# Optimization experiments

Measured on AMD Instinct MI355X. Metric: run time of the kernel, lower is better.

Reference implementation:

```python
import jax, jax.numpy as jnp
import numpy as np

N = 20000
E = 320000
IN_C = 256
HID = 64
OUT_C = 64
NUM_LAYERS = 3
HEADS = 8


def setup_inputs() -> dict:
    key = jax.random.key(0)
    ks = jax.random.split(key, 12)
    s_in = 1.0 / np.sqrt(IN_C)
    s_h = 1.0 / np.sqrt(HID)
    inp = {
        "x": jax.random.normal(ks[0], (N, IN_C), dtype=jnp.float32),
        "edge_index": jax.random.randint(ks[1], (2, E), 0, N, dtype=jnp.int64),
        "lin1_w": jax.random.uniform(ks[2], (IN_C, HID), jnp.float32, -s_in, s_in),
        "lin1_b": jnp.zeros((HID,), jnp.float32),
        "wq": jax.random.uniform(ks[3], (NUM_LAYERS, HID, HID), jnp.float32, -s_h, s_h),
        "bq": jnp.zeros((NUM_LAYERS, HID), jnp.float32),
        "wk": jax.random.uniform(ks[4], (NUM_LAYERS, HID, HID), jnp.float32, -s_h, s_h),
        "bk": jnp.zeros((NUM_LAYERS, HID), jnp.float32),
        "wv": jax.random.uniform(ks[5], (NUM_LAYERS, HID, HID), jnp.float32, -s_h, s_h),
        "bv": jnp.zeros((NUM_LAYERS, HID), jnp.float32),
        "lin2_w": jax.random.uniform(ks[6], (HID, OUT_C), jnp.float32, -s_h, s_h),
        "lin2_b": jnp.zeros((OUT_C,), jnp.float32),
    }
    return inp


def reference(x, edge_index, lin1_w, lin1_b, wq, bq, wk, bk, wv, bv, lin2_w, lin2_b):
    n = x.shape[0]
    C = lin1_w.shape[1]
    d = C // HEADS  # per-head dim
    inv_sqrt_d = 1.0 / (d ** 0.5)

    # gcn_norm with self-loops (symmetric normalization, edge weights = 1)
    loop = jnp.arange(n, dtype=edge_index.dtype)
    row = jnp.concatenate([edge_index[0], loop])  # source j
    col = jnp.concatenate([edge_index[1], loop])  # target i
    deg = jax.ops.segment_sum(jnp.ones_like(col, dtype=x.dtype), col, num_segments=n)
    dinv = jnp.where(deg > 0, deg ** -0.5, 0.0)
    norm = dinv[row] * dinv[col]  # [E+N]

    # input projection (dropout inactive in eval mode)
    h = jax.nn.relu(x @ lin1_w + lin1_b)
    x_all = h[:, None, :]  # [N, 1, C] growing history

    for l in range(NUM_LAYERS):
        t = x_all.shape[1]
        # node-level projections (linear commutes with gather)
        q = x_all[:, -1] @ wq[l] + bq[l]                      # [N, C]
        k = jnp.einsum("ntc,cd->ntd", x_all, wk[l]) + bk[l]   # [N, t, C]
        v = jnp.einsum("ntc,cd->ntd", x_all, wv[l]) + bv[l]   # [N, t, C]
        # per-edge multi-head attention of target's latest repr over source history
        Qe = q[col].reshape(-1, HEADS, d)                      # [E', H, d]
        Ke = k[row].reshape(-1, t, HEADS, d)                   # [E', t, H, d]
        Ve = v[row].reshape(-1, t, HEADS, d)
        scores = jnp.einsum("ehd,ethd->eht", Qe, Ke) * inv_sqrt_d
        attn = jax.nn.softmax(scores, axis=-1)                 # [E', H, t]
        msg = jnp.einsum("eht,ethd->ehd", attn, Ve).reshape(-1, C)
        msg = msg * norm[:, None]
        out = jax.ops.segment_sum(msg, col, num_segments=n)    # sum aggregation
        out = jax.nn.relu(out)
        x_all = jnp.concatenate([x_all, out[:, None, :]], axis=1)

    logits = x_all[:, -1] @ lin2_w + lin2_b
    return jax.nn.log_softmax(logits, axis=1)
```

## Files before the change

### kernel.cpp

```cpp
#include <hip/hip_runtime.h>
#include <math.h>

#define HID 64
#define HEADS 8
#define NUM_LAYERS 3

__device__ __forceinline__ unsigned short f2bf(float f) {
    union { float f; unsigned int u; } cv; cv.f = f;
    unsigned int u = cv.u;
    unsigned int r = (u + 0x7FFFu + ((u >> 16) & 1u)) >> 16;
    return (unsigned short)r;
}
__device__ __forceinline__ float bflo(unsigned int u) {
    union { unsigned int u; float f; } cv; cv.u = u << 16; return cv.f;
}
__device__ __forceinline__ float bfhi(unsigned int u) {
    union { unsigned int u; float f; } cv; cv.u = u & 0xFFFF0000u; return cv.f;
}

__global__ void k_count(const int* __restrict__ col, int* __restrict__ counts, int E) {
    int e = blockIdx.x * blockDim.x + threadIdx.x;
    if (e < E) atomicAdd(&counts[col[e]], 1);
}

__global__ __launch_bounds__(1024) void k_scan(const int* __restrict__ counts,
                                               int* __restrict__ start,
                                               float* __restrict__ dinv, int n) {
    __shared__ int wsum[16];
    __shared__ int carry_s;
    int tid = threadIdx.x;
    int lane = tid & 63, wv = tid >> 6;
    if (tid == 0) carry_s = 0;
    __syncthreads();
    for (int base = 0; base < n; base += 1024) {
        int i = base + tid;
        int v = (i < n) ? counts[i] : 0;
        int x = v;
#pragma unroll
        for (int off = 1; off < 64; off <<= 1) {
            int y = __shfl_up(x, off);
            if (lane >= off) x += y;
        }
        if (lane == 63) wsum[wv] = x;
        __syncthreads();
        if (wv == 0 && lane < 16) {
            int s = wsum[lane];
#pragma unroll
            for (int off = 1; off < 16; off <<= 1) {
                int y = __shfl_up(s, off);
                if (lane >= off) s += y;
            }
            wsum[lane] = s;
        }
        __syncthreads();
        int waveoff = (wv > 0) ? wsum[wv - 1] : 0;
        int carry = carry_s;
        if (i < n) {
            start[i] = carry + waveoff + x - v;
            dinv[i] = rsqrtf((float)(v + 1));
        }
        __syncthreads();
        if (tid == 0) carry_s = carry + wsum[15];
        __syncthreads();
    }
    if (threadIdx.x == 0) start[n] = carry_s;
}

__global__ void k_scatter(const int* __restrict__ ei, const int* __restrict__ start,
                          int* __restrict__ fill, int* __restrict__ ebuf, int E) {
    int e = blockIdx.x * blockDim.x + threadIdx.x;
    if (e >= E) return;
    int r = ei[e], c = ei[E + e];
    int pos = start[c] + atomicAdd(&fill[c], 1);
    ebuf[pos] = r;
}

#define ST_STRIDE 68

__device__ __forceinline__ void gemm_tile_stage_src(
    float* st, const float* __restrict__ src, int node0, int n, int ld,
    int kc, bool relu_in, int tid) {
    int nd = tid >> 4;
    int c4 = (tid & 15) * 4;
#pragma unroll
    for (int rep = 0; rep < 4; ++rep) {
        int lnode = nd + rep * 16;
        int node = node0 + lnode;
        float4 v = make_float4(0.f, 0.f, 0.f, 0.f);
        if (node < n) v = *(const float4*)&src[(size_t)node * ld + kc + c4];
        if (relu_in) {
            v.x = fmaxf(v.x, 0.f); v.y = fmaxf(v.y, 0.f);
            v.z = fmaxf(v.z, 0.f); v.w = fmaxf(v.w, 0.f);
        }
        st[(c4 + 0) * ST_STRIDE + lnode] = v.x;
        st[(c4 + 1) * ST_STRIDE + lnode] = v.y;
        st[(c4 + 2) * ST_STRIDE + lnode] = v.z;
        st[(c4 + 3) * ST_STRIDE + lnode] = v.w;
    }
}

__device__ __forceinline__ void gemm_tile_inner(
    const float* st, const float* wl, int ri, int j, float acc[4][4]) {
#pragma unroll 4
    for (int c = 0; c < 64; ++c) {
        float4 a  = *(const float4*)&st[c * ST_STRIDE + ri * 4];
        float4 b4 = *(const float4*)&wl[c * 64 + j * 4];
        acc[0][0] += a.x * b4.x; acc[0][1] += a.x * b4.y;
        acc[0][2] += a.x * b4.z; acc[0][3] += a.x * b4.w;
        acc[1][0] += a.y * b4.x; acc[1][1] += a.y * b4.y;
        acc[1][2] += a.y * b4.z; acc[1][3] += a.y * b4.w;
        acc[2][0] += a.z * b4.x; acc[2][1] += a.z * b4.y;
        acc[2][2] += a.z * b4.z; acc[2][3] += a.z * b4.w;
        acc[3][0] += a.w * b4.x; acc[3][1] += a.w * b4.y;
        acc[3][2] += a.w * b4.z; acc[3][3] += a.w * b4.w;
    }
}

__global__ __launch_bounds__(256, 4) void k_lin1(const float* __restrict__ x,
                                                 const float* __restrict__ w,
                                                 const float* __restrict__ b,
                                                 float* __restrict__ h, int n) {
    __shared__ float wl[64 * 64];
    __shared__ float st[64 * ST_STRIDE];
    int tid = threadIdx.x;
    int node0 = blockIdx.x * 64;
    int ri = tid >> 4, j = tid & 15;
    float acc[4][4];
#pragma unroll
    for (int m = 0; m < 4; ++m)
#pragma unroll
        for (int k = 0; k < 4; ++k) acc[m][k] = 0.f;

    for (int kc = 0; kc < 256; kc += 64) {
        for (int i = tid * 4; i < 4096; i += 1024)
            *(float4*)&wl[i] = *(const float4*)&w[kc * 64 + i];
        gemm_tile_stage_src(st, x, node0, n, 256, kc, false, tid);
        __syncthreads();
        gemm_tile_inner(st, wl, ri, j, acc);
        __syncthreads();
    }
    float4 bb = *(const float4*)&b[j * 4];
#pragma unroll
    for (int m = 0; m < 4; ++m) {
        int node = node0 + ri * 4 + m;
        if (node < n) {
            float4 o = make_float4(fmaxf(acc[m][0] + bb.x, 0.f),
                                   fmaxf(acc[m][1] + bb.y, 0.f),
                                   fmaxf(acc[m][2] + bb.z, 0.f),
                                   fmaxf(acc[m][3] + bb.w, 0.f));
            *(float4*)&h[(size_t)node * 64 + j * 4] = o;
        }
    }
}

__global__ __launch_bounds__(256, 4) void k_qkv(
    const float* __restrict__ xsbase,
    const float* __restrict__ wq, const float* __restrict__ bq,
    const float* __restrict__ wk, const float* __restrict__ bk,
    const float* __restrict__ wv, const float* __restrict__ bv,
    float* __restrict__ q, unsigned short* __restrict__ kv,
    int n, int layer, int t, int job_offset, int kv_stride) {
    int job = blockIdx.y + job_offset;
    const float* src; const float* w; const float* b; bool relu_in;
    int kv_off = 0;
    if (job == 0) {
        src = xsbase + (size_t)layer * n * 64;
        w = wq + layer * 4096; b = bq + layer * 64;
        relu_in = (layer >= 1);
    } else if (job <= t) {
        int s = job - 1;
        src = xsbase + (size_t)s * n * 64;
        w = wk + layer * 4096; b = bk + layer * 64;
        kv_off = s * 128;
        relu_in = (s >= 1);
    } else {
        int s = job - t - 1;
        src = xsbase + (size_t)s * n * 64;
        w = wv + layer * 4096; b = bv + layer * 64;
        kv_off = (t == 1) ? 0 : s * 128 + 64;
        relu_in = (s >= 1);
    }
    __shared__ float wl[64 * 64];
    __shared__ float st[64 * ST_STRIDE];
    int tid = threadIdx.x;
    int node0 = blockIdx.x * 64;
    for (int i = tid * 4; i < 4096; i += 1024)
        *(float4*)&wl[i] = *(const float4*)&w[i];
    gemm_tile_stage_src(st, src, node0, n, 64, 0, relu_in, tid);
    __syncthreads();
    int ri = tid >> 4, j = tid & 15;
    float acc[4][4];
#pragma unroll
    for (int m = 0; m < 4; ++m)
#pragma unroll
        for (int k = 0; k < 4; ++k) acc[m][k] = 0.f;
    gemm_tile_inner(st, wl, ri, j, acc);
    float4 bb = *(const float4*)&b[j * 4];
    if (job == 0) {
#pragma unroll
        for (int m = 0; m < 4; ++m) {
            int node = node0 + ri * 4 + m;
            if (node < n) {
                float4 o = make_float4(acc[m][0] + bb.x, acc[m][1] + bb.y,
                                       acc[m][2] + bb.z, acc[m][3] + bb.w);
                *(float4*)&q[(size_t)node * 64 + j * 4] = o;
            }
        }
    } else {
#pragma unroll
        for (int m = 0; m < 4; ++m) {
            int node = node0 + ri * 4 + m;
            if (node < n) {
                ushort4 o;
                o.x = f2bf(acc[m][0] + bb.x);
                o.y = f2bf(acc[m][1] + bb.y);
                o.z = f2bf(acc[m][2] + bb.z);
                o.w = f2bf(acc[m][3] + bb.w);
                *(ushort4*)&kv[(size_t)node * kv_stride + kv_off + j * 4] = o;
            }
        }
    }
}

template <int T>
__global__ __launch_bounds__(256) void k_attn_g(
    const int* __restrict__ start, const int* __restrict__ ebuf,
    const float* __restrict__ dinv, const float* __restrict__ q,
    const unsigned short* __restrict__ kv, float* __restrict__ outp, int n) {
    const int KVS = (T == 1) ? 64 : T * 128;
    int node = (int)((blockIdx.x * (size_t)blockDim.x + threadIdx.x) >> 6);
    int lane = threadIdx.x & 63;
    if (node >= n) return;
    int g = lane >> 3;
    int cb = (lane & 7) * 8;
    const float isd = 0.35355339059327373f;

    float qv[8];
    if (T > 1) {
        float4 q0 = *(const float4*)&q[(size_t)node * 64 + cb];
        float4 q1 = *(const float4*)&q[(size_t)node * 64 + cb + 4];
        qv[0] = q0.x; qv[1] = q0.y; qv[2] = q0.z; qv[3] = q0.w;
        qv[4] = q1.x; qv[5] = q1.y; qv[6] = q1.z; qv[7] = q1.w;
    }
    float dc = dinv[node];
    int s0 = start[node];
    int cnt = start[node + 1] - s0 + 1;

    float acc[8];
#pragma unroll
    for (int k = 0; k < 8; ++k) acc[k] = 0.f;

    for (int base = 0; base < cnt; base += 8) {
        int idx = base + g;
        bool valid = idx < cnt;
        int r = node;
        if (valid && idx > 0) r = ebuf[s0 + idx - 1];
        float dr = valid ? dinv[r] : 0.f;
        const unsigned short* rkv = kv + (size_t)r * KVS;

        float sc[T];
        float wgt;
        if (T > 1) {
            float m = -1e30f;
#pragma unroll
            for (int s = 0; s < T; ++s) {
                uint4 ku = *(const uint4*)&rkv[s * 128 + cb];
                float p = qv[0] * bflo(ku.x) + qv[1] * bfhi(ku.x)
                        + qv[2] * bflo(ku.y) + qv[3] * bfhi(ku.y)
                        + qv[4] * bflo(ku.z) + qv[5] * bfhi(ku.z)
                        + qv[6] * bflo(ku.w) + qv[7] * bfhi(ku.w);
                p *= isd;
                sc[s] = p;
                m = fmaxf(m, p);
            }
            float denom = 0.f;
#pragma unroll
            for (int s = 0; s < T; ++s) { sc[s] = __expf(sc[s] - m); denom += sc[s]; }
            wgt = dr / denom;
        } else {
            sc[0] = 1.f;
            wgt = dr;
        }

        float mg[8];
#pragma unroll
        for (int k = 0; k < 8; ++k) mg[k] = 0.f;
#pragma unroll
        for (int s = 0; s < T; ++s) {
            uint4 vu = *(const uint4*)&rkv[((T == 1) ? 0 : s * 128 + 64) + cb];
            float wv_ = sc[s];
            mg[0] += wv_ * bflo(vu.x); mg[1] += wv_ * bfhi(vu.x);
            mg[2] += wv_ * bflo(vu.y); mg[3] += wv_ * bfhi(vu.y);
            mg[4] += wv_ * bflo(vu.z); mg[5] += wv_ * bfhi(vu.z);
            mg[6] += wv_ * bflo(vu.w); mg[7] += wv_ * bfhi(vu.w);
        }
#pragma unroll
        for (int k = 0; k < 8; ++k) acc[k] += wgt * mg[k];
    }

#pragma unroll
    for (int off = 8; off < 64; off <<= 1) {
#pragma unroll
        for (int k = 0; k < 8; ++k) acc[k] += __shfl_xor(acc[k], off);
    }
    if (g == 0) {
        float4 o0 = make_float4(acc[0] * dc, acc[1] * dc, acc[2] * dc, acc[3] * dc);
        float4 o1 = make_float4(acc[4] * dc, acc[5] * dc, acc[6] * dc, acc[7] * dc);
        *(float4*)&outp[(size_t)node * 64 + cb] = o0;
        *(float4*)&outp[(size_t)node * 64 + cb + 4] = o1;
    }
}

__global__ __launch_bounds__(256) void k_final(
    const float* __restrict__ x3, const float* __restrict__ w,
    const float* __restrict__ b, float* __restrict__ outp, int n) {
    int wid  = (int)((blockIdx.x * (size_t)blockDim.x + threadIdx.x) >> 6);
    int lane = threadIdx.x & 63;
    if (wid >= n) return;
    float xv = fmaxf(x3[(size_t)wid * 64 + lane], 0.f);
    float acc = b[lane];
#pragma unroll
    for (int c = 0; c < 64; ++c) {
        float xc = __shfl(xv, c);
        acc += xc * w[c * 64 + lane];
    }
    float m = acc;
    for (int off = 1; off < 64; off <<= 1) m = fmaxf(m, __shfl_xor(m, off));
    float e = __expf(acc - m);
    float ssum = e;
    for (int off = 1; off < 64; off <<= 1) ssum += __shfl_xor(ssum, off);
    outp[(size_t)wid * 64 + lane] = acc - m - __logf(ssum);
}

extern "C" void kernel_launch(void* const* d_in, const int* in_sizes, int n_in,
                              void* d_out, int out_size, void* d_ws, size_t ws_size,
                              hipStream_t stream) {
    const float* x  = (const float*)d_in[0];
    const int*   ei = (const int*)d_in[1];
    const float* w1 = (const float*)d_in[2];
    const float* b1 = (const float*)d_in[3];
    const float* wq = (const float*)d_in[4];
    const float* bq = (const float*)d_in[5];
    const float* wk = (const float*)d_in[6];
    const float* bk = (const float*)d_in[7];
    const float* wv = (const float*)d_in[8];
    const float* bv = (const float*)d_in[9];
    const float* w2 = (const float*)d_in[10];
    const float* b2 = (const float*)d_in[11];
    float* outp = (float*)d_out;

    int n = in_sizes[0] / 256;
    int E = in_sizes[1] / 2;

    float* ws = (float*)d_ws;
    size_t off = 0;
    float* dinv = ws + off; off += (size_t)n;
    float* q    = ws + off; off += (size_t)n * 64;
    float* xs   = ws + off; off += (size_t)n * 64 * (NUM_LAYERS + 1);
    unsigned short* kvU = (unsigned short*)(ws + off); off += (size_t)n * 192;
    int* wsI    = (int*)(ws + off);
    int* counts = wsI;
    int* fill   = wsI + n;
    int* startA = wsI + 2 * n;
    int* ebuf   = wsI + 3 * n + 1;

    hipMemsetAsync(counts, 0, 2 * (size_t)n * sizeof(int), stream);
    k_count<<<(E + 255) / 256, 256, 0, stream>>>(ei + E, counts, E);
    k_scan<<<1, 1024, 0, stream>>>(counts, startA, dinv, n);
    k_scatter<<<(E + 255) / 256, 256, 0, stream>>>(ei, startA, fill, ebuf, E);

    k_lin1<<<(n + 63) / 64, 256, 0, stream>>>(x, w1, b1, xs, n);

    int attn_grid = (int)(((size_t)n * 64 + 255) / 256);
    for (int l = 0; l < NUM_LAYERS; ++l) {
        int t = l + 1;
        int job_offset = (l == 0) ? 2 : 0;
        int njobs      = (l == 0) ? 1 : 1 + 2 * t;
        int kv_stride  = (t == 1) ? 64 : t * 128;
        dim3 grid((n + 63) / 64, njobs);
        k_qkv<<<grid, 256, 0, stream>>>(xs, wq, bq, wk, bk, wv, bv,
                                        q, kvU, n, l, t, job_offset, kv_stride);
        float* dst = xs + (size_t)(l + 1) * n * 64;
        if (t == 1)
            k_attn_g<1><<<attn_grid, 256, 0, stream>>>(startA, ebuf, dinv, q, kvU, dst, n);
        else if (t == 2)
            k_attn_g<2><<<attn_grid, 256, 0, stream>>>(startA, ebuf, dinv, q, kvU, dst, n);
        else
            k_attn_g<3><<<attn_grid, 256, 0, stream>>>(startA, ebuf, dinv, q, kvU, dst, n);
    }

    k_final<<<((int)(((long long)n * 64 + 255) / 256)), 256, 0, stream>>>(
        xs + (size_t)NUM_LAYERS * n * 64, w2, b2, outp, n);
}
```

Baseline: 297.2 us.

## Use bf16 MFMA for linear projections and store node history in bf16

Replaces the scalar fp32 LDS-tiled GEMMs in lin1 and the QKV projection with bf16 MFMA 16x16x32 instructions, staging weights transposed in LDS as bf16. The per-layer node history buffer is now stored as bf16 instead of fp32, which halves its read and write traffic in the attention, QKV and final kernels. ReLU on the input is applied directly to packed bf16 values. The risk is lost precision from rounding inputs, weights and hidden states to bf16, and the epilogue now does scalar strided stores instead of vector stores.

```diff
diff --git a/kernel.cpp b/kernel.cpp
--- a/kernel.cpp
+++ b/kernel.cpp
@@ -4,6 +4,9 @@
 #define HID 64
 #define HEADS 8
 #define NUM_LAYERS 3
+
+typedef __attribute__((ext_vector_type(8))) short bf16x8;
+typedef __attribute__((ext_vector_type(4))) float f32x4;
 
 __device__ __forceinline__ unsigned short f2bf(float f) {
     union { float f; unsigned int u; } cv; cv.f = f;
@@ -16,6 +19,11 @@
 }
 __device__ __forceinline__ float bfhi(unsigned int u) {
     union { unsigned int u; float f; } cv; cv.u = u & 0xFFFF0000u; return cv.f;
+}
+__device__ __forceinline__ unsigned relu_pk(unsigned u) {
+    unsigned m = ((u & 0x8000u) ? 0u : 0xFFFFu) |
+                 ((u & 0x80000000u) ? 0u : 0xFFFF0000u);
+    return u & m;
 }
 
 __global__ void k_count(const int* __restrict__ col, int* __restrict__ counts, int E) {
@@ -75,93 +83,94 @@
     ebuf[pos] = r;
 }
 
-#define ST_STRIDE 68
-
-__device__ __forceinline__ void gemm_tile_stage_src(
-    float* st, const float* __restrict__ src, int node0, int n, int ld,
-    int kc, bool relu_in, int tid) {
-    int nd = tid >> 4;
-    int c4 = (tid & 15) * 4;
-#pragma unroll
-    for (int rep = 0; rep < 4; ++rep) {
-        int lnode = nd + rep * 16;
-        int node = node0 + lnode;
-        float4 v = make_float4(0.f, 0.f, 0.f, 0.f);
-        if (node < n) v = *(const float4*)&src[(size_t)node * ld + kc + c4];
-        if (relu_in) {
-            v.x = fmaxf(v.x, 0.f); v.y = fmaxf(v.y, 0.f);
-            v.z = fmaxf(v.z, 0.f); v.w = fmaxf(v.w, 0.f);
-        }
-        st[(c4 + 0) * ST_STRIDE + lnode] = v.x;
-        st[(c4 + 1) * ST_STRIDE + lnode] = v.y;
-        st[(c4 + 2) * ST_STRIDE + lnode] = v.z;
-        st[(c4 + 3) * ST_STRIDE + lnode] = v.w;
-    }
-}
-
-__device__ __forceinline__ void gemm_tile_inner(
-    const float* st, const float* wl, int ri, int j, float acc[4][4]) {
-#pragma unroll 4
-    for (int c = 0; c < 64; ++c) {
-        float4 a  = *(const float4*)&st[c * ST_STRIDE + ri * 4];
-        float4 b4 = *(const float4*)&wl[c * 64 + j * 4];
-        acc[0][0] += a.x * b4.x; acc[0][1] += a.x * b4.y;
-        acc[0][2] += a.x * b4.z; acc[0][3] += a.x * b4.w;
-        acc[1][0] += a.y * b4.x; acc[1][1] += a.y * b4.y;
-        acc[1][2] += a.y * b4.z; acc[1][3] += a.y * b4.w;
-        acc[2][0] += a.z * b4.x; acc[2][1] += a.z * b4.y;
-        acc[2][2] += a.z * b4.z; acc[2][3] += a.z * b4.w;
-        acc[3][0] += a.w * b4.x; acc[3][1] += a.w * b4.y;
-        acc[3][2] += a.w * b4.z; acc[3][3] += a.w * b4.w;
+#define ALD 72
+
+__device__ __forceinline__ void stage_w_bf16(unsigned short* Wt,
+                                             const float* __restrict__ w, int tid) {
+    for (int idx = tid; idx < 1024; idx += 256) {
+        int k = idx >> 4, n4 = (idx & 15) * 4;
+        float4 wv = *(const float4*)&w[k * 64 + n4];
+        Wt[(n4 + 0) * ALD + k] = f2bf(wv.x);
+        Wt[(n4 + 1) * ALD + k] = f2bf(wv.y);
+        Wt[(n4 + 2) * ALD + k] = f2bf(wv.z);
+        Wt[(n4 + 3) * ALD + k] = f2bf(wv.w);
+    }
+}
+
+__device__ __forceinline__ void mfma_step(const unsigned short* Alds,
+                                          const unsigned short* Wt,
+                                          int tid, f32x4 acc[4]) {
+    int lane = tid & 63;
+    int m0 = (tid >> 6) * 16;
+    int c16 = lane & 15, quad = lane >> 4;
+    const unsigned short* ar = &Alds[(m0 + c16) * ALD + quad * 8];
+    bf16x8 a0 = *(const bf16x8*)ar;
+    bf16x8 a1 = *(const bf16x8*)(ar + 32);
+#pragma unroll
+    for (int nt = 0; nt < 4; ++nt) {
+        const unsigned short* br = &Wt[(nt * 16 + c16) * ALD + quad * 8];
+        bf16x8 b0 = *(const bf16x8*)br;
+        bf16x8 b1 = *(const bf16x8*)(br + 32);
+        acc[nt] = __builtin_amdgcn_mfma_f32_16x16x32_bf16(a0, b0, acc[nt], 0, 0, 0);
+        acc[nt] = __builtin_amdgcn_mfma_f32_16x16x32_bf16(a1, b1, acc[nt], 0, 0, 0);
     }
 }
 
 __global__ __launch_bounds__(256, 4) void k_lin1(const float* __restrict__ x,
                                                  const float* __restrict__ w,
                                                  const float* __restrict__ b,
-                                                 float* __restrict__ h, int n) {
-    __shared__ float wl[64 * 64];
-    __shared__ float st[64 * ST_STRIDE];
+                                                 unsigned short* __restrict__ h, int n) {
+    __shared__ __align__(16) unsigned short Alds[64 * ALD];
+    __shared__ __align__(16) unsigned short Wt[64 * ALD];
     int tid = threadIdx.x;
     int node0 = blockIdx.x * 64;
-    int ri = tid >> 4, j = tid & 15;
-    float acc[4][4];
-#pragma unroll
-    for (int m = 0; m < 4; ++m)
-#pragma unroll
-        for (int k = 0; k < 4; ++k) acc[m][k] = 0.f;
+    f32x4 acc[4];
+#pragma unroll
+    for (int nt = 0; nt < 4; ++nt) acc[nt] = (f32x4){0.f, 0.f, 0.f, 0.f};
 
     for (int kc = 0; kc < 256; kc += 64) {
-        for (int i = tid * 4; i < 4096; i += 1024)
-            *(float4*)&wl[i] = *(const float4*)&w[kc * 64 + i];
-        gemm_tile_stage_src(st, x, node0, n, 256, kc, false, tid);
-        __syncthreads();
-        gemm_tile_inner(st, wl, ri, j, acc);
-        __syncthreads();
-    }
-    float4 bb = *(const float4*)&b[j * 4];
-#pragma unroll
-    for (int m = 0; m < 4; ++m) {
-        int node = node0 + ri * 4 + m;
+        __syncthreads();
+        stage_w_bf16(Wt, w + kc * 64, tid);
+        for (int idx = tid; idx < 1024; idx += 256) {
+            int r = idx >> 4, c4 = (idx & 15) * 4;
+            int node = node0 + r;
+            float4 v = make_float4(0.f, 0.f, 0.f, 0.f);
+            if (node < n) v = *(const float4*)&x[(size_t)node * 256 + kc + c4];
+            Alds[r * ALD + c4 + 0] = f2bf(v.x);
+            Alds[r * ALD + c4 + 1] = f2bf(v.y);
+            Alds[r * ALD + c4 + 2] = f2bf(v.z);
+            Alds[r * ALD + c4 + 3] = f2bf(v.w);
+        }
+        __syncthreads();
+        mfma_step(Alds, Wt, tid, acc);
+    }
+    int lane = tid & 63;
+    int m0 = (tid >> 6) * 16, c16 = lane & 15, quad = lane >> 4;
+    float bias[4];
+#pragma unroll
+    for (int nt = 0; nt < 4; ++nt) bias[nt] = b[nt * 16 + c16];
+#pragma unroll
+    for (int i = 0; i < 4; ++i) {
+        int node = node0 + m0 + quad * 4 + i;
         if (node < n) {
-            float4 o = make_float4(fmaxf(acc[m][0] + bb.x, 0.f),
-                                   fmaxf(acc[m][1] + bb.y, 0.f),
-                                   fmaxf(acc[m][2] + bb.z, 0.f),
-                                   fmaxf(acc[m][3] + bb.w, 0.f));
-            *(float4*)&h[(size_t)node * 64 + j * 4] = o;
+#pragma unroll
+            for (int nt = 0; nt < 4; ++nt) {
+                float o = acc[nt][i] + bias[nt];
+                h[(size_t)node * 64 + nt * 16 + c16] = f2bf(fmaxf(o, 0.f));
+            }
         }
     }
 }
 
 __global__ __launch_bounds__(256, 4) void k_qkv(
-    const float* __restrict__ xsbase,
+    const unsigned short* __restrict__ xsbase,
     const float* __restrict__ wq, const float* __restrict__ bq,
     const float* __restrict__ wk, const float* __restrict__ bk,
     const float* __restrict__ wv, const float* __restrict__ bv,
     float* __restrict__ q, unsigned short* __restrict__ kv,
     int n, int layer, int t, int job_offset, int kv_stride) {
     int job = blockIdx.y + job_offset;
-    const float* src; const float* w; const float* b; bool relu_in;
+    const unsigned short* src; const float* w; const float* b; bool relu_in;
     int kv_off = 0;
     if (job == 0) {
         src = xsbase + (size_t)layer * n * 64;
@@ -180,43 +189,52 @@
         kv_off = (t == 1) ? 0 : s * 128 + 64;
         relu_in = (s >= 1);
     }
-    __shared__ float wl[64 * 64];
-    __shared__ float st[64 * ST_STRIDE];
+    __shared__ __align__(16) unsigned short Alds[64 * ALD];
+    __shared__ __align__(16) unsigned short Wt[64 * ALD];
     int tid = threadIdx.x;
     int node0 = blockIdx.x * 64;
-    for (int i = tid * 4; i < 4096; i += 1024)
-        *(float4*)&wl[i] = *(const float4*)&w[i];
-    gemm_tile_stage_src(st, src, node0, n, 64, 0, relu_in, tid);
+    stage_w_bf16(Wt, w, tid);
+    for (int idx = tid; idx < 512; idx += 256) {
+        int r = idx >> 3, seg = idx & 7;
+        int node = node0 + r;
+        uint4 u = make_uint4(0u, 0u, 0u, 0u);
+        if (node < n) u = *(const uint4*)&src[(size_t)node * 64 + seg * 8];
+        if (relu_in) {
+            u.x = relu_pk(u.x); u.y = relu_pk(u.y);
+            u.z = relu_pk(u.z); u.w = relu_pk(u.w);
+        }
+        *(uint4*)&Alds[r * ALD + seg * 8] = u;
+    }
     __syncthreads();
-    int ri = tid >> 4, j = tid & 15;
-    float acc[4][4];
-#pragma unroll
-    for (int m = 0; m < 4; ++m)
-#pragma unroll
-        for (int k = 0; k < 4; ++k) acc[m][k] = 0.f;
-    gemm_tile_inner(st, wl, ri, j, acc);
-    float4 bb = *(const float4*)&b[j * 4];
+    f32x4 acc[4];
+#pragma unroll
+    for (int nt = 0; nt < 4; ++nt) acc[nt] = (f32x4){0.f, 0.f, 0.f, 0.f};
+    mfma_step(Alds, Wt, tid, acc);
+
+    int lane = tid & 63;
+    int m0 = (tid >> 6) * 16, c16 = lane & 15, quad = lane >> 4;
+    float bias[4];
+#pragma unroll
+    for (int nt = 0; nt < 4; ++nt) bias[nt] = b[nt * 16 + c16];
     if (job == 0) {
 #pragma unroll
-        for (int m = 0; m < 4; ++m) {
-            int node = node0 + ri * 4 + m;
+        for (int i = 0; i < 4; ++i) {
+            int node = node0 + m0 + quad * 4 + i;
             if (node < n) {
-                float4 o = make_float4(acc[m][0] + bb.x, acc[m][1] + bb.y,
-                                       acc[m][2] + bb.z, acc[m][3] + bb.w);
-                *(float4*)&q[(size_t)node * 64 + j * 4] = o;
+#pragma unroll
+                for (int nt = 0; nt < 4; ++nt)
+                    q[(size_t)node * 64 + nt * 16 + c16] = acc[nt][i] + bias[nt];
             }
         }
     } else {
 #pragma unroll
-        for (int m = 0; m < 4; ++m) {
-            int node = node0 + ri * 4 + m;
+        for (int i = 0; i < 4; ++i) {
+            int node = node0 + m0 + quad * 4 + i;
             if (node < n) {
-                ushort4 o;
-                o.x = f2bf(acc[m][0] + bb.x);
-                o.y = f2bf(acc[m][1] + bb.y);
-                o.z = f2bf(acc[m][2] + bb.z);
-                o.w = f2bf(acc[m][3] + bb.w);
-                *(ushort4*)&kv[(size_t)node * kv_stride + kv_off + j * 4] = o;
+#pragma unroll
+                for (int nt = 0; nt < 4; ++nt)
+                    kv[(size_t)node * kv_stride + kv_off + nt * 16 + c16] =
+                        f2bf(acc[nt][i] + bias[nt]);
             }
         }
     }
@@ -226,7 +244,7 @@
 __global__ __launch_bounds__(256) void k_attn_g(
     const int* __restrict__ start, const int* __restrict__ ebuf,
     const float* __restrict__ dinv, const float* __restrict__ q,
-    const unsigned short* __restrict__ kv, float* __restrict__ outp, int n) {
+    const unsigned short* __restrict__ kv, unsigned short* __restrict__ outp, int n) {
     const int KVS = (T == 1) ? 64 : T * 128;
     int node = (int)((blockIdx.x * (size_t)blockDim.x + threadIdx.x) >> 6);
     int lane = threadIdx.x & 63;
@@ -304,20 +322,23 @@
         for (int k = 0; k < 8; ++k) acc[k] += __shfl_xor(acc[k], off);
     }
     if (g == 0) {
-        float4 o0 = make_float4(acc[0] * dc, acc[1] * dc, acc[2] * dc, acc[3] * dc);
-        float4 o1 = make_float4(acc[4] * dc, acc[5] * dc, acc[6] * dc, acc[7] * dc);
-        *(float4*)&outp[(size_t)node * 64 + cb] = o0;
-        *(float4*)&outp[(size_t)node * 64 + cb + 4] = o1;
+        ushort4 o0, o1;
+        o0.x = f2bf(acc[0] * dc); o0.y = f2bf(acc[1] * dc);
+        o0.z = f2bf(acc[2] * dc); o0.w = f2bf(acc[3] * dc);
+        o1.x = f2bf(acc[4] * dc); o1.y = f2bf(acc[5] * dc);
+        o1.z = f2bf(acc[6] * dc); o1.w = f2bf(acc[7] * dc);
+        *(ushort4*)&outp[(size_t)node * 64 + cb] = o0;
+        *(ushort4*)&outp[(size_t)node * 64 + cb + 4] = o1;
     }
 }
 
 __global__ __launch_bounds__(256) void k_final(
-    const float* __restrict__ x3, const float* __restrict__ w,
+    const unsigned short* __restrict__ x3, const float* __restrict__ w,
     const float* __restrict__ b, float* __restrict__ outp, int n) {
     int wid  = (int)((blockIdx.x * (size_t)blockDim.x + threadIdx.x) >> 6);
     int lane = threadIdx.x & 63;
     if (wid >= n) return;
-    float xv = fmaxf(x3[(size_t)wid * 64 + lane], 0.f);
+    float xv = fmaxf(bflo((unsigned)x3[(size_t)wid * 64 + lane]), 0.f);
     float acc = b[lane];
 #pragma unroll
     for (int c = 0; c < 64; ++c) {
@@ -356,7 +377,7 @@
     size_t off = 0;
     float* dinv = ws + off; off += (size_t)n;
     float* q    = ws + off; off += (size_t)n * 64;
-    float* xs   = ws + off; off += (size_t)n * 64 * (NUM_LAYERS + 1);
+    unsigned short* xsU = (unsigned short*)(ws + off); off += (size_t)n * 128;
     unsigned short* kvU = (unsigned short*)(ws + off); off += (size_t)n * 192;
     int* wsI    = (int*)(ws + off);
     int* counts = wsI;
@@ -369,7 +390,7 @@
     k_scan<<<1, 1024, 0, stream>>>(counts, startA, dinv, n);
     k_scatter<<<(E + 255) / 256, 256, 0, stream>>>(ei, startA, fill, ebuf, E);
 
-    k_lin1<<<(n + 63) / 64, 256, 0, stream>>>(x, w1, b1, xs, n);
+    k_lin1<<<(n + 63) / 64, 256, 0, stream>>>(x, w1, b1, xsU, n);
 
     int attn_grid = (int)(((size_t)n * 64 + 255) / 256);
     for (int l = 0; l < NUM_LAYERS; ++l) {
@@ -378,9 +399,9 @@
         int njobs      = (l == 0) ? 1 : 1 + 2 * t;
         int kv_stride  = (t == 1) ? 64 : t * 128;
         dim3 grid((n + 63) / 64, njobs);
-        k_qkv<<<grid, 256, 0, stream>>>(xs, wq, bq, wk, bk, wv, bv,
+        k_qkv<<<grid, 256, 0, stream>>>(xsU, wq, bq, wk, bk, wv, bv,
                                         q, kvU, n, l, t, job_offset, kv_stride);
-        float* dst = xs + (size_t)(l + 1) * n * 64;
+        unsigned short* dst = xsU + (size_t)(l + 1) * n * 64;
         if (t == 1)
             k_attn_g<1><<<attn_grid, 256, 0, stream>>>(startA, ebuf, dinv, q, kvU, dst, n);
         else if (t == 2)
@@ -390,5 +411,5 @@
     }
 
     k_final<<<((int)(((long long)n * 64 + 255) / 256)), 256, 0, stream>>>(
-        xs + (size_t)NUM_LAYERS * n * 64, w2, b2, outp, n);
-}
+        xsU + (size_t)NUM_LAYERS * n * 64, w2, b2, outp, n);
+}
```

After: 267.3 us. 1.11x faster.
